# Optimization experiments

Hardware: AMD Instinct MI355X
Metric: run time of the kernel (lower is better)

Reference implementation:

```python
import jax, jax.numpy as jnp
import numpy as np

B, D_IN, D_OUT, N_SUBNET, G = 16384, 512, 512, 8, 2


def setup_inputs() -> dict:
    key = jax.random.key(0)
    k_x, k_g, k_w = jax.random.split(key, 3)
    x = jax.random.normal(k_x, (B, D_IN), dtype=jnp.float32)
    groups = jax.random.randint(k_g, (B, G), 0, N_SUBNET, dtype=jnp.int32)
    # per-expert Dense params (the 'subnets')
    W = jax.random.normal(k_w, (N_SUBNET, D_IN, D_OUT), dtype=jnp.float32) * (1.0 / np.sqrt(D_IN))
    b = jnp.zeros((N_SUBNET, D_OUT), dtype=jnp.float32)
    return {"x": x, "groups": groups, "W": W, "b": b}


def reference(x, groups, W, b):
    """SubnetGate: one-hot gated dispatch to per-group subnets + combine.

    Faithful math: gates = one_hot(groups[:, group_col], n_subnet);
    out = sum_e gates[:, e] * subnet_e(x). Since gates are one-hot the
    combine selects exactly one expert output per row (gate weight 1.0).
    """
    group_col = 0
    n_subnet = W.shape[0]
    idx_group = groups[:, group_col]                     # [B]
    gates = jax.nn.one_hot(idx_group, n_subnet, dtype=x.dtype)  # [B, E]
    # run every expert on the full batch (dense reference for the
    # gather-compute-scatter kernel), then gate-combine
    expert_out = jnp.einsum("bi,eio->beo", x, W) + b[None, :, :]  # [B, E, O]
    out = jnp.einsum("be,beo->bo", gates, expert_out)             # [B, O]
    return out
```

## Files before the change

kernel.cpp:

```cpp
#include <hip/hip_runtime.h>
#include <hip/hip_bf16.h>


#define NROWS   16384
#define KDIM    512
#define NDIM    512
#define NEXP    8
#define BM      128
#define BN      128
#define BK      64
#define NT_PER  4
#define KT_PER  8
#define TILE_ELEMS (BN * BK)
#define WS_ROWLIST_OFF 4096
#define WS_WT_OFF      (4096 + NEXP * NROWS * 4)

typedef __bf16        bf16x8 __attribute__((ext_vector_type(8)));
typedef float         f32x4  __attribute__((ext_vector_type(4)));
typedef unsigned int  u32x4  __attribute__((ext_vector_type(4)));

__device__ __forceinline__ unsigned int f2bf_u(float f) {
    unsigned int u = __builtin_bit_cast(unsigned int, f);
    return (u + 0x7FFFu + ((u >> 16) & 1u)) >> 16;
}

__device__ __forceinline__ void gl_lds16(const void* g, void* l) {
    __builtin_amdgcn_global_load_lds(
        (const __attribute__((address_space(1))) unsigned int*)g,
        (__attribute__((address_space(3))) unsigned int*)l, 16, 0, 0);
}

__global__ void zero_kernel(int* __restrict__ gcnt) {
    if (threadIdx.x < NEXP) gcnt[threadIdx.x] = 0;
}

__global__ void prep_kernel(const float* __restrict__ W,
                            const int* __restrict__ groups,
                            int* __restrict__ gcnt,
                            int* __restrict__ rowlist,
                            unsigned short* __restrict__ Wtile) {
    __shared__ __align__(16) unsigned short tl[TILE_ELEMS];
    __shared__ int lcnt[NEXP];
    __shared__ int lbase[NEXP];
    const int bid = blockIdx.x;
    const int tid = threadIdx.x;

    if (bid < 256) {
        const int e  = bid >> 5;
        const int nt = (bid >> 3) & 3;
        const int kt = bid & 7;
        const float* Wb = W + (size_t)e * (KDIM * NDIM);
        #pragma unroll
        for (int i = 0; i < 4; ++i) {
            int f = i * 256 + tid;
            int n = f & 127;
            int g = f >> 7;
            int col = nt * BN + n;
            unsigned int p[4];
            #pragma unroll
            for (int jj = 0; jj < 4; ++jj) {
                int k0 = kt * BK + g * 8 + jj * 2;
                unsigned int lo = f2bf_u(Wb[(size_t)k0 * NDIM + col]);
                unsigned int hi = f2bf_u(Wb[(size_t)(k0 + 1) * NDIM + col]);
                p[jj] = lo | (hi << 16);
            }
            *(u32x4*)&tl[n * 64 + (g ^ (n & 7)) * 8] = *(const u32x4*)p;
        }
        __syncthreads();
        unsigned short* dst = Wtile + (size_t)bid * TILE_ELEMS;
        #pragma unroll
        for (int i = 0; i < 4; ++i) {
            int off = (i * 256 + tid) * 8;
            *(u32x4*)&dst[off] = *(const u32x4*)&tl[off];
        }
    } else {
        const int base = (bid - 256) * 256;
        if (tid < NEXP) lcnt[tid] = 0;
        __syncthreads();
        int r = base + tid;
        int e = groups[r * 2];
        int pos = atomicAdd(&lcnt[e], 1);
        __syncthreads();
        if (tid < NEXP) lbase[tid] = atomicAdd(&gcnt[tid], lcnt[tid]);
        __syncthreads();
        rowlist[e * NROWS + lbase[e] + pos] = r;
    }
}

__global__ __launch_bounds__(256, 2)
void gemm_kernel(const float* __restrict__ x,
                 const int* __restrict__ counts,
                 const int* __restrict__ rowlist,
                 const unsigned short* __restrict__ Wtile,
                 const float* __restrict__ bias,
                 float* __restrict__ out) {
    __shared__ __align__(16) unsigned short Asm[BM * 72];
    __shared__ __align__(16) unsigned short Bsm[TILE_ELEMS];

    const int bid = blockIdx.x;
    const int e   = bid >> 9;
    const int mt  = (bid >> 2) & 127;
    const int nt  = bid & 3;
    const int cnt = counts[e];
    const int rb  = mt * BM;
    if (rb >= cnt) return;
    int m_valid = cnt - rb;
    if (m_valid > BM) m_valid = BM;
    const int* rl = rowlist + e * NROWS + rb;

    const int tid = threadIdx.x;
    const int w   = tid >> 6;
    const int ln  = tid & 63;
    const int q   = ln >> 4;
    const int l15 = ln & 15;
    const int wm  = (w >> 1) * 64;
    const int wn  = (w & 1) * 64;

    const float* srcp[4];
    #pragma unroll
    for (int i = 0; i < 4; ++i) {
        int f = i * 256 + tid;
        int m = f >> 3;
        int g = f & 7;
        srcp[i] = (m < m_valid) ? (x + (size_t)rl[m] * KDIM + g * 8) : nullptr;
    }

    const unsigned short* wt =
        Wtile + (size_t)((e * NT_PER + nt) * KT_PER) * TILE_ELEMS;

    f32x4 acc[4][4];
    #pragma unroll
    for (int mi = 0; mi < 4; ++mi)
        #pragma unroll
        for (int ni = 0; ni < 4; ++ni)
            acc[mi][ni] = (f32x4){0.f, 0.f, 0.f, 0.f};

    for (int kt = 0; kt < KT_PER; ++kt) {
        const unsigned short* wsrc = wt + (size_t)kt * TILE_ELEMS;
        #pragma unroll
        for (int i = 0; i < 4; ++i) {
            int off = (i * 256 + tid) * 8;
            gl_lds16(wsrc + off, &Bsm[off]);
        }
        #pragma unroll
        for (int i = 0; i < 4; ++i) {
            int f = i * 256 + tid;
            int m = f >> 3;
            int g = f & 7;
            u32x4 pack = {0u, 0u, 0u, 0u};
            if (srcp[i]) {
                const float* s = srcp[i] + kt * BK;
                f32x4 f0 = *(const f32x4*)s;
                f32x4 f1 = *(const f32x4*)(s + 4);
                pack.x = f2bf_u(f0.x) | (f2bf_u(f0.y) << 16);
                pack.y = f2bf_u(f0.z) | (f2bf_u(f0.w) << 16);
                pack.z = f2bf_u(f1.x) | (f2bf_u(f1.y) << 16);
                pack.w = f2bf_u(f1.z) | (f2bf_u(f1.w) << 16);
            }
            *(u32x4*)&Asm[m * 72 + g * 8] = pack;
        }
        __syncthreads();
        #pragma unroll
        for (int ks = 0; ks < 2; ++ks) {
            const int g = ks * 4 + q;
            bf16x8 af[4], bf[4];
            #pragma unroll
            for (int mi = 0; mi < 4; ++mi)
                af[mi] = *(const bf16x8*)&Asm[(wm + mi * 16 + l15) * 72 + g * 8];
            #pragma unroll
            for (int ni = 0; ni < 4; ++ni) {
                int n = wn + ni * 16 + l15;
                bf[ni] = *(const bf16x8*)&Bsm[n * 64 + (g ^ (n & 7)) * 8];
            }
            #pragma unroll
            for (int mi = 0; mi < 4; ++mi)
                #pragma unroll
                for (int ni = 0; ni < 4; ++ni)
                    acc[mi][ni] = __builtin_amdgcn_mfma_f32_16x16x32_bf16(
                        af[mi], bf[ni], acc[mi][ni], 0, 0, 0);
        }
        __syncthreads();
    }

    int growv[16];
    #pragma unroll
    for (int mi = 0; mi < 4; ++mi)
        #pragma unroll
        for (int r = 0; r < 4; ++r) {
            int rloc = wm + mi * 16 + q * 4 + r;
            growv[mi * 4 + r] = (rloc < m_valid) ? rl[rloc] : -1;
        }
    const int ncol0 = nt * BN + wn;
    #pragma unroll
    for (int ni = 0; ni < 4; ++ni) {
        int col = ncol0 + ni * 16 + l15;
        float bv = bias[e * NDIM + col];
        #pragma unroll
        for (int mi = 0; mi < 4; ++mi)
            #pragma unroll
            for (int r = 0; r < 4; ++r) {
                int gr = growv[mi * 4 + r];
                if (gr >= 0) out[(size_t)gr * NDIM + col] = acc[mi][ni][r] + bv;
            }
    }
}

extern "C" void kernel_launch(void* const* d_in, const int* in_sizes, int n_in,
                              void* d_out, int out_size, void* d_ws, size_t ws_size,
                              hipStream_t stream) {
    const float* x      = (const float*)d_in[0];
    const int*   groups = (const int*)d_in[1];
    const float* W      = (const float*)d_in[2];
    const float* b      = (const float*)d_in[3];
    float*       out    = (float*)d_out;

    char* ws = (char*)d_ws;
    int*            counts  = (int*)ws;
    int*            rowlist = (int*)(ws + WS_ROWLIST_OFF);
    unsigned short* Wtile   = (unsigned short*)(ws + WS_WT_OFF);

    zero_kernel<<<1, 64, 0, stream>>>(counts);
    prep_kernel<<<320, 256, 0, stream>>>(W, groups, counts, rowlist, Wtile);
    gemm_kernel<<<4096, 256, 0, stream>>>(x, counts, rowlist, Wtile, b, out);
}
```

Baseline: 127.4 us.

## Pre-gather activations into bf16 swizzled tiles and run compacted persistent GEMM

Adds a plan kernel that builds a compact list of (expert, 64-row tile) descriptors, and a gather kernel that converts gathered x rows to bf16 in swizzled tile layout. The new GEMM streams both A and B tiles straight into LDS through global_load_lds, uses 64-row tiles and occupancy 4, and loops grid-stride over the compact tile list. This is meant to remove in-loop fp32 loads and conversion plus the empty blocks of the old 4096-block grid. The cost is two extra kernel launches and a round trip of the gathered bf16 activations through workspace memory. The old kernel is kept as a fallback when the workspace is too small.

After: 131.1 us. 1.03x slower.

```diff
diff --git a/kernel.cpp b/kernel.cpp
--- a/kernel.cpp
+++ b/kernel.cpp
@@ -6,14 +6,15 @@
 #define KDIM    512
 #define NDIM    512
 #define NEXP    8
-#define BM      128
-#define BN      128
-#define BK      64
-#define NT_PER  4
-#define KT_PER  8
-#define TILE_ELEMS (BN * BK)
+#define TILE_ELEMS 8192
+#define ATILE_ELEMS 4096
+#define MAX_DESC 264
+#define WS_NDESC_OFF   64
+#define WS_DESC_OFF    128
 #define WS_ROWLIST_OFF 4096
 #define WS_WT_OFF      (4096 + NEXP * NROWS * 4)
+#define WS_XG_OFF      (WS_WT_OFF + NEXP * KDIM * NDIM * 2)
+#define WS_NEED        ((size_t)WS_XG_OFF + (size_t)MAX_DESC * 8 * ATILE_ELEMS * 2)
 
 typedef __bf16        bf16x8 __attribute__((ext_vector_type(8)));
 typedef float         f32x4  __attribute__((ext_vector_type(4)));
@@ -23,7 +24,15 @@
     unsigned int u = __builtin_bit_cast(unsigned int, f);
     return (u + 0x7FFFu + ((u >> 16) & 1u)) >> 16;
 }
-
+__device__ __forceinline__ unsigned int pack2(float a, float b) {
+    return f2bf_u(a) | (f2bf_u(b) << 16);
+}
+__device__ __forceinline__ u32x4 pack8(f32x4 a, f32x4 b) {
+    u32x4 p;
+    p.x = pack2(a.x, a.y); p.y = pack2(a.z, a.w);
+    p.z = pack2(b.x, b.y); p.w = pack2(b.z, b.w);
+    return p;
+}
 __device__ __forceinline__ void gl_lds16(const void* g, void* l) {
     __builtin_amdgcn_global_load_lds(
         (const __attribute__((address_space(1))) unsigned int*)g,
@@ -55,14 +64,13 @@
             int f = i * 256 + tid;
             int n = f & 127;
             int g = f >> 7;
-            int col = nt * BN + n;
+            int col = nt * 128 + n;
             unsigned int p[4];
             #pragma unroll
             for (int jj = 0; jj < 4; ++jj) {
-                int k0 = kt * BK + g * 8 + jj * 2;
-                unsigned int lo = f2bf_u(Wb[(size_t)k0 * NDIM + col]);
-                unsigned int hi = f2bf_u(Wb[(size_t)(k0 + 1) * NDIM + col]);
-                p[jj] = lo | (hi << 16);
+                int k0 = kt * 64 + g * 8 + jj * 2;
+                p[jj] = pack2(Wb[(size_t)k0 * NDIM + col],
+                              Wb[(size_t)(k0 + 1) * NDIM + col]);
             }
             *(u32x4*)&tl[n * 64 + (g ^ (n & 7)) * 8] = *(const u32x4*)p;
         }
@@ -87,14 +95,178 @@
     }
 }
 
+__global__ void plan_kernel(const int* __restrict__ counts,
+                            int* __restrict__ ndesc,
+                            int* __restrict__ desc) {
+    if (threadIdx.x == 0) {
+        int M = 0;
+        for (int e = 0; e < NEXP; ++e) {
+            int nmt = (counts[e] + 63) >> 6;
+            for (int mt = 0; mt < nmt && M < MAX_DESC; ++mt)
+                desc[M++] = (e << 16) | mt;
+        }
+        ndesc[0] = M;
+    }
+}
+
+__global__ __launch_bounds__(256, 4)
+void gather_kernel(const float* __restrict__ x,
+                   const int* __restrict__ counts,
+                   const int* __restrict__ rowlist,
+                   const int* __restrict__ ndesc,
+                   const int* __restrict__ desc,
+                   unsigned short* __restrict__ xg) {
+    const int bid = blockIdx.x;
+    const int d  = bid >> 3;
+    const int kt = bid & 7;
+    if (d >= ndesc[0]) return;
+    const int de = desc[d];
+    const int e  = de >> 16;
+    const int mt = de & 0xffff;
+    const int cnt = counts[e];
+    int m_valid = cnt - mt * 64;
+    if (m_valid > 64) m_valid = 64;
+    const int* rl = rowlist + e * NROWS + mt * 64;
+
+    const int t = threadIdx.x;
+    const int m = t >> 2;
+    const int c = t & 3;
+
+    u32x4 lo = {0u,0u,0u,0u}, hi = {0u,0u,0u,0u};
+    if (m < m_valid) {
+        const float* s = x + (size_t)rl[m] * KDIM + kt * 64 + c * 16;
+        f32x4 v0 = *(const f32x4*)(s);
+        f32x4 v1 = *(const f32x4*)(s + 4);
+        f32x4 v2 = *(const f32x4*)(s + 8);
+        f32x4 v3 = *(const f32x4*)(s + 12);
+        lo = pack8(v0, v1);
+        hi = pack8(v2, v3);
+    }
+    const int p = m & 7;
+    unsigned short* tile = xg + ((size_t)d * 8 + kt) * ATILE_ELEMS;
+    int base = (m * 8 + ((2 * c) ^ (p & 6))) * 8;
+    if (p & 1) {
+        *(u32x4*)&tile[base]     = hi;
+        *(u32x4*)&tile[base + 8] = lo;
+    } else {
+        *(u32x4*)&tile[base]     = lo;
+        *(u32x4*)&tile[base + 8] = hi;
+    }
+}
+
+__global__ __launch_bounds__(256, 4)
+void gemm_tiled(const unsigned short* __restrict__ xg,
+                const int* __restrict__ counts,
+                const int* __restrict__ rowlist,
+                const unsigned short* __restrict__ Wtile,
+                const float* __restrict__ bias,
+                float* __restrict__ out,
+                const int* __restrict__ ndesc,
+                const int* __restrict__ desc) {
+    __shared__ __align__(16) unsigned short Asm[ATILE_ELEMS];
+    __shared__ __align__(16) unsigned short Bsm[TILE_ELEMS];
+
+    const int tid = threadIdx.x;
+    const int w   = tid >> 6;
+    const int ln  = tid & 63;
+    const int q   = ln >> 4;
+    const int l15 = ln & 15;
+    const int wm  = (w >> 1) * 32;
+    const int wn  = (w & 1) * 64;
+
+    const int T = ndesc[0] * 4;
+    for (int tix = blockIdx.x; tix < T; tix += gridDim.x) {
+        const int d  = tix >> 2;
+        const int nt = tix & 3;
+        const int de = desc[d];
+        const int e  = de >> 16;
+        const int mt = de & 0xffff;
+        const int cnt = counts[e];
+        int m_valid = cnt - mt * 64;
+        if (m_valid > 64) m_valid = 64;
+        const int* rl = rowlist + e * NROWS + mt * 64;
+
+        const unsigned short* atile = xg + (size_t)d * 8 * ATILE_ELEMS;
+        const unsigned short* btile = Wtile + (size_t)(e * 32 + nt * 8) * TILE_ELEMS;
+
+        f32x4 acc[2][4];
+        #pragma unroll
+        for (int mi = 0; mi < 2; ++mi)
+            #pragma unroll
+            for (int ni = 0; ni < 4; ++ni)
+                acc[mi][ni] = (f32x4){0.f, 0.f, 0.f, 0.f};
+
+        #pragma unroll 1
+        for (int kt = 0; kt < 8; ++kt) {
+            const unsigned short* asrc = atile + kt * ATILE_ELEMS;
+            const unsigned short* bsrc = btile + kt * TILE_ELEMS;
+            #pragma unroll
+            for (int i = 0; i < 2; ++i) {
+                int off = (i * 256 + tid) * 8;
+                gl_lds16(asrc + off, &Asm[off]);
+            }
+            #pragma unroll
+            for (int i = 0; i < 4; ++i) {
+                int off = (i * 256 + tid) * 8;
+                gl_lds16(bsrc + off, &Bsm[off]);
+            }
+            __syncthreads();
+            #pragma unroll
+            for (int ks = 0; ks < 2; ++ks) {
+                const int g = ks * 4 + q;
+                bf16x8 af[2], bfr[4];
+                #pragma unroll
+                for (int mi = 0; mi < 2; ++mi) {
+                    int r = wm + mi * 16 + l15;
+                    af[mi] = *(const bf16x8*)&Asm[(r * 8 + (g ^ (r & 7))) * 8];
+                }
+                #pragma unroll
+                for (int ni = 0; ni < 4; ++ni) {
+                    int n = wn + ni * 16 + l15;
+                    bfr[ni] = *(const bf16x8*)&Bsm[n * 64 + (g ^ (n & 7)) * 8];
+                }
+                #pragma unroll
+                for (int mi = 0; mi < 2; ++mi)
+                    #pragma unroll
+                    for (int ni = 0; ni < 4; ++ni)
+                        acc[mi][ni] = __builtin_amdgcn_mfma_f32_16x16x32_bf16(
+                            af[mi], bfr[ni], acc[mi][ni], 0, 0, 0);
+            }
+            __syncthreads();
+        }
+
+        int growv[8];
+        #pragma unroll
+        for (int mi = 0; mi < 2; ++mi)
+            #pragma unroll
+            for (int r = 0; r < 4; ++r) {
+                int rloc = wm + mi * 16 + q * 4 + r;
+                growv[mi * 4 + r] = (rloc < m_valid) ? rl[rloc] : -1;
+            }
+        const int ncol0 = nt * 128 + wn;
+        #pragma unroll
+        for (int ni = 0; ni < 4; ++ni) {
+            int col = ncol0 + ni * 16 + l15;
+            float bv = bias[e * NDIM + col];
+            #pragma unroll
+            for (int mi = 0; mi < 2; ++mi)
+                #pragma unroll
+                for (int r = 0; r < 4; ++r) {
+                    int gr = growv[mi * 4 + r];
+                    if (gr >= 0) out[(size_t)gr * NDIM + col] = acc[mi][ni][r] + bv;
+                }
+        }
+    }
+}
+
 __global__ __launch_bounds__(256, 2)
-void gemm_kernel(const float* __restrict__ x,
-                 const int* __restrict__ counts,
-                 const int* __restrict__ rowlist,
-                 const unsigned short* __restrict__ Wtile,
-                 const float* __restrict__ bias,
-                 float* __restrict__ out) {
-    __shared__ __align__(16) unsigned short Asm[BM * 72];
+void gemm_fb(const float* __restrict__ x,
+             const int* __restrict__ counts,
+             const int* __restrict__ rowlist,
+             const unsigned short* __restrict__ Wtile,
+             const float* __restrict__ bias,
+             float* __restrict__ out) {
+    __shared__ __align__(16) unsigned short Asm[128 * 72];
     __shared__ __align__(16) unsigned short Bsm[TILE_ELEMS];
 
     const int bid = blockIdx.x;
@@ -102,10 +274,10 @@
     const int mt  = (bid >> 2) & 127;
     const int nt  = bid & 3;
     const int cnt = counts[e];
-    const int rb  = mt * BM;
+    const int rb  = mt * 128;
     if (rb >= cnt) return;
     int m_valid = cnt - rb;
-    if (m_valid > BM) m_valid = BM;
+    if (m_valid > 128) m_valid = 128;
     const int* rl = rowlist + e * NROWS + rb;
 
     const int tid = threadIdx.x;
@@ -117,16 +289,16 @@
     const int wn  = (w & 1) * 64;
 
     const float* srcp[4];
+    int lm[4], lg[4];
     #pragma unroll
     for (int i = 0; i < 4; ++i) {
         int f = i * 256 + tid;
-        int m = f >> 3;
-        int g = f & 7;
-        srcp[i] = (m < m_valid) ? (x + (size_t)rl[m] * KDIM + g * 8) : nullptr;
-    }
-
-    const unsigned short* wt =
-        Wtile + (size_t)((e * NT_PER + nt) * KT_PER) * TILE_ELEMS;
+        lm[i] = f >> 3;
+        lg[i] = f & 7;
+        srcp[i] = (lm[i] < m_valid) ? (x + (size_t)rl[lm[i]] * KDIM + lg[i] * 8)
+                                    : nullptr;
+    }
+    const unsigned short* wt = Wtile + (size_t)(e * 32 + nt * 8) * TILE_ELEMS;
 
     f32x4 acc[4][4];
     #pragma unroll
@@ -135,7 +307,7 @@
         for (int ni = 0; ni < 4; ++ni)
             acc[mi][ni] = (f32x4){0.f, 0.f, 0.f, 0.f};
 
-    for (int kt = 0; kt < KT_PER; ++kt) {
+    for (int kt = 0; kt < 8; ++kt) {
         const unsigned short* wsrc = wt + (size_t)kt * TILE_ELEMS;
         #pragma unroll
         for (int i = 0; i < 4; ++i) {
@@ -144,40 +316,32 @@
         }
         #pragma unroll
         for (int i = 0; i < 4; ++i) {
-            int f = i * 256 + tid;
-            int m = f >> 3;
-            int g = f & 7;
-            u32x4 pack = {0u, 0u, 0u, 0u};
+            u32x4 p = {0u, 0u, 0u, 0u};
             if (srcp[i]) {
-                const float* s = srcp[i] + kt * BK;
-                f32x4 f0 = *(const f32x4*)s;
-                f32x4 f1 = *(const f32x4*)(s + 4);
-                pack.x = f2bf_u(f0.x) | (f2bf_u(f0.y) << 16);
-                pack.y = f2bf_u(f0.z) | (f2bf_u(f0.w) << 16);
-                pack.z = f2bf_u(f1.x) | (f2bf_u(f1.y) << 16);
-                pack.w = f2bf_u(f1.z) | (f2bf_u(f1.w) << 16);
-            }
-            *(u32x4*)&Asm[m * 72 + g * 8] = pack;
+                const float* s = srcp[i] + kt * 64;
+                p = pack8(*(const f32x4*)s, *(const f32x4*)(s + 4));
+            }
+            *(u32x4*)&Asm[lm[i] * 72 + lg[i] * 8] = p;
         }
         __syncthreads();
         #pragma unroll
         for (int ks = 0; ks < 2; ++ks) {
             const int g = ks * 4 + q;
-            bf16x8 af[4], bf[4];
+            bf16x8 af[4], bfr[4];
             #pragma unroll
             for (int mi = 0; mi < 4; ++mi)
                 af[mi] = *(const bf16x8*)&Asm[(wm + mi * 16 + l15) * 72 + g * 8];
             #pragma unroll
             for (int ni = 0; ni < 4; ++ni) {
                 int n = wn + ni * 16 + l15;
-                bf[ni] = *(const bf16x8*)&Bsm[n * 64 + (g ^ (n & 7)) * 8];
+                bfr[ni] = *(const bf16x8*)&Bsm[n * 64 + (g ^ (n & 7)) * 8];
             }
             #pragma unroll
             for (int mi = 0; mi < 4; ++mi)
                 #pragma unroll
                 for (int ni = 0; ni < 4; ++ni)
                     acc[mi][ni] = __builtin_amdgcn_mfma_f32_16x16x32_bf16(
-                        af[mi], bf[ni], acc[mi][ni], 0, 0, 0);
+                        af[mi], bfr[ni], acc[mi][ni], 0, 0, 0);
         }
         __syncthreads();
     }
@@ -190,7 +354,7 @@
             int rloc = wm + mi * 16 + q * 4 + r;
             growv[mi * 4 + r] = (rloc < m_valid) ? rl[rloc] : -1;
         }
-    const int ncol0 = nt * BN + wn;
+    const int ncol0 = nt * 128 + wn;
     #pragma unroll
     for (int ni = 0; ni < 4; ++ni) {
         int col = ncol0 + ni * 16 + l15;
@@ -216,10 +380,21 @@
 
     char* ws = (char*)d_ws;
     int*            counts  = (int*)ws;
+    int*            ndesc   = (int*)(ws + WS_NDESC_OFF);
+    int*            desc    = (int*)(ws + WS_DESC_OFF);
     int*            rowlist = (int*)(ws + WS_ROWLIST_OFF);
     unsigned short* Wtile   = (unsigned short*)(ws + WS_WT_OFF);
+    unsigned short* xg      = (unsigned short*)(ws + WS_XG_OFF);
 
     zero_kernel<<<1, 64, 0, stream>>>(counts);
     prep_kernel<<<320, 256, 0, stream>>>(W, groups, counts, rowlist, Wtile);
-    gemm_kernel<<<4096, 256, 0, stream>>>(x, counts, rowlist, Wtile, b, out);
-}
+    plan_kernel<<<1, 64, 0, stream>>>(counts, ndesc, desc);
+    if (ws_size >= WS_NEED) {
+        gather_kernel<<<MAX_DESC * 8, 256, 0, stream>>>(x, counts, rowlist,
+                                                        ndesc, desc, xg);
+        gemm_tiled<<<MAX_DESC * 4, 256, 0, stream>>>(xg, counts, rowlist,
+                                                     Wtile, b, out, ndesc, desc);
+    } else {
+        gemm_fb<<<4096, 256, 0, stream>>>(x, counts, rowlist, Wtile, b, out);
+    }
+}
```
